# Performance work log

Measured on AMD Instinct MI355X. Metric: run time of the kernel, lower is better.

The kernel has to match this reference:

```python
import jax, jax.numpy as jnp
import numpy as np

REG_TOPK = 4
REG_CHANNELS = 64
ADD_MEAN = True
TOTAL_DIM = REG_TOPK + (1 if ADD_MEAN else 0)  # 5


def setup_inputs() -> dict:
    key = jax.random.key(0)
    k1, k2, k3 = jax.random.split(key, 3)
    N, C, H, W = 32, 32, 160, 160  # C = 4*(reg_max+1), reg_max=7
    x = jax.random.normal(k1, (N, C, H, W), dtype=jnp.float32)
    # 1x1 conv params, init std=0.01, bias 0 (as in torch module)
    w1 = jax.random.normal(k2, (REG_CHANNELS, 4 * TOTAL_DIM), dtype=jnp.float32) * 0.01
    b1 = jnp.zeros((REG_CHANNELS,), dtype=jnp.float32)
    w2 = jax.random.normal(k3, (1, REG_CHANNELS), dtype=jnp.float32) * 0.01
    b2 = jnp.zeros((1,), dtype=jnp.float32)
    return {"x": x, "w1": w1, "b1": b1, "w2": w2, "b2": b2}


def reference(x, w1, b1, w2, b2):
    N, C, H, W = x.shape
    bins = C // 4
    # softmax over distribution bins; move bins to last axis for top_k
    p = jax.nn.softmax(x.reshape(N, 4, bins, H, W), axis=2)  # (N,4,bins,H,W)
    p = jnp.transpose(p, (0, 1, 3, 4, 2))                    # (N,4,H,W,bins)
    topk, _ = jax.lax.top_k(p, REG_TOPK)                     # (N,4,H,W,k)
    if ADD_MEAN:
        stat = jnp.concatenate([topk, topk.mean(axis=-1, keepdims=True)], axis=-1)
    else:
        stat = topk                                          # (N,4,H,W,total_dim)
    # reshape to (N, 4*total_dim, H, W) matching torch layout (4, total_dim contiguous)
    stat = jnp.transpose(stat, (0, 1, 4, 2, 3)).reshape(N, 4 * TOTAL_DIM, H, W)
    y = jax.nn.relu(jnp.einsum('nchw,oc->nohw', stat, w1) + b1[None, :, None, None])
    y = jax.nn.sigmoid(jnp.einsum('nchw,oc->nohw', y, w2) + b2[None, :, None, None])
    return y
```

## Files before the change

kernel.cpp:

```cpp
#include <hip/hip_runtime.h>

#define HW_ 25600
#define CHW_ (32 * 25600)
#define NPIX 819200
#define ROWB 40

typedef short bf16x8 __attribute__((ext_vector_type(8)));
typedef float f32x4 __attribute__((ext_vector_type(4)));

__device__ __forceinline__ unsigned short f2bf(float f) {
    unsigned int u = __float_as_uint(f);
    return (unsigned short)((u + 0x7FFFu + ((u >> 16) & 1u)) >> 16);
}

__global__ void dgqp_prep(const float* __restrict__ w1,
                          const float* __restrict__ b1,
                          unsigned short* __restrict__ w1f) {
    int t = threadIdx.x;
    int lane = t & 63;
    int col = ((t >> 6) << 4) | (lane & 15);
    int kg = lane >> 4;
    unsigned int pk[4];
    #pragma unroll
    for (int pr = 0; pr < 4; ++pr) {
        unsigned short hh[2];
        #pragma unroll
        for (int e = 0; e < 2; ++e) {
            int k = kg * 8 + pr * 2 + e;
            float v = 0.f;
            if (k < 16) {
                int g = k >> 2, idx = k & 3;
                v = w1[col * 20 + g * 5 + idx] + 0.25f * w1[col * 20 + g * 5 + 4];
            } else if (k == 16) {
                v = b1[col];
            }
            hh[e] = f2bf(v);
        }
        pk[pr] = (unsigned int)hh[0] | ((unsigned int)hh[1] << 16);
    }
    *reinterpret_cast<uint4*>(w1f + t * 8) = make_uint4(pk[0], pk[1], pk[2], pk[3]);
}

__global__ __launch_bounds__(256) void dgqp_main(
    const float* __restrict__ x,
    const unsigned short* __restrict__ w1f,
    const float* __restrict__ w2,
    const float* __restrict__ b2,
    float* __restrict__ out)
{
    __shared__ unsigned short lds[256 * ROWB];

    const int tid  = threadIdx.x;
    const int lane = tid & 63;
    const int wb   = tid & 192;
    const int q    = lane & 15;
    const int kg   = lane >> 4;
    const int px   = blockIdx.x * 256 + tid;
    const unsigned int n = (unsigned int)px / HW_;
    const unsigned int off = (unsigned int)px + n * (unsigned int)(CHW_ - HW_);
    const float* xp = x + off;

    unsigned int hp[8];

#define PROC(g, buf) do {                                                   \
        float sum = 0.f, t0 = 0.f, t1 = 0.f, t2 = 0.f, t3 = 0.f;            \
        _Pragma("unroll")                                                   \
        for (int b = 0; b < 8; ++b) {                                       \
            float e = __expf(buf[b]);                                       \
            sum += e;                                                       \
            float u0 = fminf(t0, e);  t0 = fmaxf(t0, e);                    \
            float u1 = fminf(t1, u0); t1 = fmaxf(t1, u0);                   \
            float u2 = fminf(t2, u1); t2 = fmaxf(t2, u1);                   \
            t3 = fmaxf(t3, u2);                                             \
        }                                                                   \
        float inv = __builtin_amdgcn_rcpf(sum);                             \
        hp[(g)*2]   = (unsigned)f2bf(t0*inv) | ((unsigned)f2bf(t1*inv)<<16);\
        hp[(g)*2+1] = (unsigned)f2bf(t2*inv) | ((unsigned)f2bf(t3*inv)<<16);\
    } while (0)

    float va[8], vb[8];
    #pragma unroll
    for (int b = 0; b < 8; ++b) va[b] = xp[(size_t)b * HW_];
    #pragma unroll
    for (int b = 0; b < 8; ++b) vb[b] = xp[(size_t)(8 + b) * HW_];
    __builtin_amdgcn_sched_barrier(0);
    PROC(0, va);
    #pragma unroll
    for (int b = 0; b < 8; ++b) va[b] = xp[(size_t)(16 + b) * HW_];
    __builtin_amdgcn_sched_barrier(0);
    PROC(1, vb);
    #pragma unroll
    for (int b = 0; b < 8; ++b) vb[b] = xp[(size_t)(24 + b) * HW_];
    __builtin_amdgcn_sched_barrier(0);
    PROC(2, va);
    __builtin_amdgcn_sched_barrier(0);
    PROC(3, vb);
#undef PROC

    unsigned short* row = lds + tid * ROWB;
    *reinterpret_cast<uint4*>(row)      = make_uint4(hp[0], hp[1], hp[2], hp[3]);
    *reinterpret_cast<uint4*>(row + 8)  = make_uint4(hp[4], hp[5], hp[6], hp[7]);
    *reinterpret_cast<uint4*>(row + 16) = make_uint4(0x3F80u, 0u, 0u, 0u);
    *reinterpret_cast<uint4*>(row + 24) = make_uint4(0u, 0u, 0u, 0u);
    __syncthreads();

    bf16x8 bfrag[4];
    #pragma unroll
    for (int nt = 0; nt < 4; ++nt)
        bfrag[nt] = *reinterpret_cast<const bf16x8*>(w1f + (nt * 64 + lane) * 8);

    float w2l[4];
    #pragma unroll
    for (int nt = 0; nt < 4; ++nt) w2l[nt] = w2[nt * 16 + q];

    const f32x4 zero4 = {0.f, 0.f, 0.f, 0.f};
    const float bb2 = b2[0];
    const int outbase = blockIdx.x * 256 + wb;

    #pragma unroll
    for (int m = 0; m < 4; ++m) {
        bf16x8 afrag = *reinterpret_cast<const bf16x8*>(
            lds + (wb + m * 16 + q) * ROWB + kg * 8);

        float pm0 = 0.f, pm1 = 0.f, pm2 = 0.f, pm3 = 0.f;
        #pragma unroll
        for (int nt = 0; nt < 4; ++nt) {
            f32x4 d = __builtin_amdgcn_mfma_f32_16x16x32_bf16(afrag, bfrag[nt], zero4, 0, 0, 0);
            pm0 = fmaf(w2l[nt], fmaxf(d[0], 0.f), pm0);
            pm1 = fmaf(w2l[nt], fmaxf(d[1], 0.f), pm1);
            pm2 = fmaf(w2l[nt], fmaxf(d[2], 0.f), pm2);
            pm3 = fmaf(w2l[nt], fmaxf(d[3], 0.f), pm3);
        }
        #pragma unroll
        for (int sh = 1; sh < 16; sh <<= 1) {
            pm0 += __shfl_xor(pm0, sh);
            pm1 += __shfl_xor(pm1, sh);
            pm2 += __shfl_xor(pm2, sh);
            pm3 += __shfl_xor(pm3, sh);
        }
        if (q < 4) {
            float r = pm0;
            if (q == 1) r = pm1;
            if (q == 2) r = pm2;
            if (q == 3) r = pm3;
            float y = __builtin_amdgcn_rcpf(1.f + __expf(-(r + bb2)));
            out[outbase + m * 16 + kg * 4 + q] = y;
        }
    }
}

extern "C" void kernel_launch(void* const* d_in, const int* in_sizes, int n_in,
                              void* d_out, int out_size, void* d_ws, size_t ws_size,
                              hipStream_t stream) {
    const float* x  = (const float*)d_in[0];
    const float* w1 = (const float*)d_in[1];
    const float* b1 = (const float*)d_in[2];
    const float* w2 = (const float*)d_in[3];
    const float* b2 = (const float*)d_in[4];
    float* out = (float*)d_out;
    unsigned short* w1f = (unsigned short*)d_ws;

    dgqp_prep<<<1, 256, 0, stream>>>(w1, b1, w1f);
    dgqp_main<<<NPIX / 256, 256, 0, stream>>>(x, w1f, w2, b2, out);
}
```

Baseline: 32.07 us.

## Process two pixels per thread with packed fp16 softmax/top-k and f16 MFMA

Each thread now loads float2 pairs of adjacent pixels. Their exponentials are converted to packed half2, so the top-4 selection, sum and normalisation run with packed fp16 min/max/add/mul, roughly halving per-pixel VALU work. The MFMA switches from bf16 to f16 operands. The LDS row shrinks to 24 halves, and the grid is halved so each block covers 512 pixels. The aim is to relieve VALU pressure in a mostly bandwidth-bound kernel and get wider loads. The cost is extra register use and lower fp16 range and accuracy for the softmax intermediates.

```diff
diff --git a/kernel.cpp b/kernel.cpp
--- a/kernel.cpp
+++ b/kernel.cpp
@@ -3,14 +3,25 @@
 #define HW_ 25600
 #define CHW_ (32 * 25600)
 #define NPIX 819200
-#define ROWB 40
+#define ROWH 24
 
-typedef short bf16x8 __attribute__((ext_vector_type(8)));
+typedef _Float16 f16x8 __attribute__((ext_vector_type(8)));
+typedef _Float16 h2 __attribute__((ext_vector_type(2)));
 typedef float f32x4 __attribute__((ext_vector_type(4)));
 
-__device__ __forceinline__ unsigned short f2bf(float f) {
-    unsigned int u = __float_as_uint(f);
-    return (unsigned short)((u + 0x7FFFu + ((u >> 16) & 1u)) >> 16);
+__device__ __forceinline__ unsigned short h2us(_Float16 h) {
+    return __builtin_bit_cast(unsigned short, h);
+}
+__device__ __forceinline__ unsigned packlo(h2 a, h2 b) {
+    h2 r = {a.x, b.x};
+    return __builtin_bit_cast(unsigned, r);
+}
+__device__ __forceinline__ unsigned packhi(h2 a, h2 b) {
+    h2 r = {a.y, b.y};
+    return __builtin_bit_cast(unsigned, r);
+}
+__device__ __forceinline__ h2 pkrtz(float a, float b) {
+    return __builtin_bit_cast(h2, __builtin_amdgcn_cvt_pkrtz(a, b));
 }
 
 __global__ void dgqp_prep(const float* __restrict__ w1,
@@ -34,7 +45,7 @@
             } else if (k == 16) {
                 v = b1[col];
             }
-            hh[e] = f2bf(v);
+            hh[e] = h2us((_Float16)v);
         }
         pk[pr] = (unsigned int)hh[0] | ((unsigned int)hh[1] << 16);
     }
@@ -48,66 +59,80 @@
     const float* __restrict__ b2,
     float* __restrict__ out)
 {
-    __shared__ unsigned short lds[256 * ROWB];
+    __shared__ _Float16 lds[512 * ROWH + 8];
 
     const int tid  = threadIdx.x;
     const int lane = tid & 63;
-    const int wb   = tid & 192;
+    const int wpb  = (tid & 192) << 1;
     const int q    = lane & 15;
     const int kg   = lane >> 4;
-    const int px   = blockIdx.x * 256 + tid;
-    const unsigned int n = (unsigned int)px / HW_;
-    const unsigned int off = (unsigned int)px + n * (unsigned int)(CHW_ - HW_);
+    const int base = (blockIdx.x * 256 + tid) * 2;
+    const unsigned int n = (unsigned int)base / HW_;
+    const unsigned int off = (unsigned int)base + n * (unsigned int)(CHW_ - HW_);
     const float* xp = x + off;
 
-    unsigned int hp[8];
+    _Float16* row0 = lds + (tid * 2) * ROWH;
+    _Float16* row1 = row0 + ROWH;
 
-#define PROC(g, buf) do {                                                   \
-        float sum = 0.f, t0 = 0.f, t1 = 0.f, t2 = 0.f, t3 = 0.f;            \
-        _Pragma("unroll")                                                   \
-        for (int b = 0; b < 8; ++b) {                                       \
-            float e = __expf(buf[b]);                                       \
-            sum += e;                                                       \
-            float u0 = fminf(t0, e);  t0 = fmaxf(t0, e);                    \
-            float u1 = fminf(t1, u0); t1 = fmaxf(t1, u0);                   \
-            float u2 = fminf(t2, u1); t2 = fmaxf(t2, u1);                   \
-            t3 = fmaxf(t3, u2);                                             \
-        }                                                                   \
-        float inv = __builtin_amdgcn_rcpf(sum);                             \
-        hp[(g)*2]   = (unsigned)f2bf(t0*inv) | ((unsigned)f2bf(t1*inv)<<16);\
-        hp[(g)*2+1] = (unsigned)f2bf(t2*inv) | ((unsigned)f2bf(t3*inv)<<16);\
+#define PROC(g, buf) do {                                                    \
+        h2 e[8];                                                             \
+        _Pragma("unroll")                                                    \
+        for (int b = 0; b < 8; ++b)                                          \
+            e[b] = pkrtz(__expf(buf[b].x), __expf(buf[b].y));                \
+        h2 t0 = (h2)0, t1 = (h2)0, t2 = (h2)0, t3 = (h2)0;                   \
+        _Pragma("unroll")                                                    \
+        for (int b = 0; b < 8; ++b) {                                        \
+            h2 u0 = __builtin_elementwise_min(t0, e[b]);                     \
+            t0    = __builtin_elementwise_max(t0, e[b]);                     \
+            h2 u1 = __builtin_elementwise_min(t1, u0);                       \
+            t1    = __builtin_elementwise_max(t1, u0);                       \
+            h2 u2 = __builtin_elementwise_min(t2, u1);                       \
+            t2    = __builtin_elementwise_max(t2, u1);                       \
+            t3    = __builtin_elementwise_max(t3, u2);                       \
+        }                                                                    \
+        h2 sum = ((e[0] + e[1]) + (e[2] + e[3])) + ((e[4] + e[5]) + (e[6] + e[7])); \
+        float ix = __builtin_amdgcn_rcpf((float)sum.x);                      \
+        float iy = __builtin_amdgcn_rcpf((float)sum.y);                      \
+        h2 inv = pkrtz(ix, iy);                                              \
+        t0 = t0 * inv; t1 = t1 * inv; t2 = t2 * inv; t3 = t3 * inv;          \
+        *reinterpret_cast<uint2*>(row0 + (g) * 4) =                          \
+            make_uint2(packlo(t0, t1), packlo(t2, t3));                      \
+        *reinterpret_cast<uint2*>(row1 + (g) * 4) =                          \
+            make_uint2(packhi(t0, t1), packhi(t2, t3));                      \
     } while (0)
 
-    float va[8], vb[8];
+    float2 va[8], vb[8];
     #pragma unroll
-    for (int b = 0; b < 8; ++b) va[b] = xp[(size_t)b * HW_];
+    for (int b = 0; b < 8; ++b)
+        va[b] = *reinterpret_cast<const float2*>(xp + (size_t)b * HW_);
     #pragma unroll
-    for (int b = 0; b < 8; ++b) vb[b] = xp[(size_t)(8 + b) * HW_];
+    for (int b = 0; b < 8; ++b)
+        vb[b] = *reinterpret_cast<const float2*>(xp + (size_t)(8 + b) * HW_);
     __builtin_amdgcn_sched_barrier(0);
     PROC(0, va);
     #pragma unroll
-    for (int b = 0; b < 8; ++b) va[b] = xp[(size_t)(16 + b) * HW_];
+    for (int b = 0; b < 8; ++b)
+        va[b] = *reinterpret_cast<const float2*>(xp + (size_t)(16 + b) * HW_);
     __builtin_amdgcn_sched_barrier(0);
     PROC(1, vb);
     #pragma unroll
-    for (int b = 0; b < 8; ++b) vb[b] = xp[(size_t)(24 + b) * HW_];
+    for (int b = 0; b < 8; ++b)
+        vb[b] = *reinterpret_cast<const float2*>(xp + (size_t)(24 + b) * HW_);
     __builtin_amdgcn_sched_barrier(0);
     PROC(2, va);
     __builtin_amdgcn_sched_barrier(0);
     PROC(3, vb);
 #undef PROC
 
-    unsigned short* row = lds + tid * ROWB;
-    *reinterpret_cast<uint4*>(row)      = make_uint4(hp[0], hp[1], hp[2], hp[3]);
-    *reinterpret_cast<uint4*>(row + 8)  = make_uint4(hp[4], hp[5], hp[6], hp[7]);
-    *reinterpret_cast<uint4*>(row + 16) = make_uint4(0x3F80u, 0u, 0u, 0u);
-    *reinterpret_cast<uint4*>(row + 24) = make_uint4(0u, 0u, 0u, 0u);
+    const uint4 tail = make_uint4(0x00003C00u, 0u, 0u, 0u);
+    *reinterpret_cast<uint4*>(row0 + 16) = tail;
+    *reinterpret_cast<uint4*>(row1 + 16) = tail;
     __syncthreads();
 
-    bf16x8 bfrag[4];
+    f16x8 bfrag[4];
     #pragma unroll
     for (int nt = 0; nt < 4; ++nt)
-        bfrag[nt] = *reinterpret_cast<const bf16x8*>(w1f + (nt * 64 + lane) * 8);
+        bfrag[nt] = *reinterpret_cast<const f16x8*>(w1f + (nt * 64 + lane) * 8);
 
     float w2l[4];
     #pragma unroll
@@ -115,17 +140,17 @@
 
     const f32x4 zero4 = {0.f, 0.f, 0.f, 0.f};
     const float bb2 = b2[0];
-    const int outbase = blockIdx.x * 256 + wb;
+    const int outbase = blockIdx.x * 512 + wpb;
 
     #pragma unroll
-    for (int m = 0; m < 4; ++m) {
-        bf16x8 afrag = *reinterpret_cast<const bf16x8*>(
-            lds + (wb + m * 16 + q) * ROWB + kg * 8);
+    for (int m = 0; m < 8; ++m) {
+        f16x8 afrag = *reinterpret_cast<const f16x8*>(
+            lds + (wpb + m * 16 + q) * ROWH + kg * 8);
 
         float pm0 = 0.f, pm1 = 0.f, pm2 = 0.f, pm3 = 0.f;
         #pragma unroll
         for (int nt = 0; nt < 4; ++nt) {
-            f32x4 d = __builtin_amdgcn_mfma_f32_16x16x32_bf16(afrag, bfrag[nt], zero4, 0, 0, 0);
+            f32x4 d = __builtin_amdgcn_mfma_f32_16x16x32_f16(afrag, bfrag[nt], zero4, 0, 0, 0);
             pm0 = fmaf(w2l[nt], fmaxf(d[0], 0.f), pm0);
             pm1 = fmaf(w2l[nt], fmaxf(d[1], 0.f), pm1);
             pm2 = fmaf(w2l[nt], fmaxf(d[2], 0.f), pm2);
@@ -161,5 +186,5 @@
     unsigned short* w1f = (unsigned short*)d_ws;
 
     dgqp_prep<<<1, 256, 0, stream>>>(w1, b1, w1f);
-    dgqp_main<<<NPIX / 256, 256, 0, stream>>>(x, w1f, w2, b2, out);
+    dgqp_main<<<NPIX / 512, 256, 0, stream>>>(x, w1f, w2, b2, out);
 }
```

Result: slower. 33.07 us (+3.1%).
